# Kernel tuning notes

Measured on AMD Instinct MI355X. Metric: run time of the kernel, lower is better.

Reference implementation:

```python
import jax, jax.numpy as jnp
import numpy as np

N = 10000          # num token nodes
E = 320000         # num token-token edges (avg degree 32)
IN_DIM = 512
FEAT_DIM = 128
OUT_DIM = 64       # per-head dim
HEADS = 8
NEG_SLOPE = 0.01   # torch F.leaky_relu default


def setup_inputs() -> dict:
    key = jax.random.key(0)
    k = jax.random.split(key, 7)
    h = jax.random.normal(k[0], (N, IN_DIM), dtype=jnp.float32)
    dep_emb = jax.random.normal(k[1], (E, FEAT_DIM), dtype=jnp.float32)
    src = jax.random.randint(k[2], (E,), 0, N, dtype=jnp.int32)
    dst = jnp.sort(jax.random.randint(k[3], (E,), 0, N, dtype=jnp.int32))
    # xavier-normal-ish init (gain for relu ~ sqrt(2))
    w_fc = jax.random.normal(k[4], (IN_DIM, OUT_DIM * HEADS), dtype=jnp.float32) * np.float32(np.sqrt(4.0 / (IN_DIM + OUT_DIM * HEADS)))
    w_feat = jax.random.normal(k[5], (FEAT_DIM, OUT_DIM * HEADS), dtype=jnp.float32) * np.float32(np.sqrt(4.0 / (FEAT_DIM + OUT_DIM * HEADS)))
    w_attn = jax.random.normal(k[6], (3 * OUT_DIM,), dtype=jnp.float32) * np.float32(np.sqrt(4.0 / (3 * OUT_DIM + 1)))
    return {"h": h, "dep_emb": dep_emb, "src": src, "dst": dst,
            "w_fc": w_fc, "w_feat": w_feat, "w_attn": w_attn}


def reference(h, dep_emb, src, dst, w_fc, w_feat, w_attn):
    # node projection: [N, H, D]
    z = (h @ w_fc).reshape(N, HEADS, OUT_DIM)
    # edge-feature projection: [E, H, D]
    feat = (dep_emb @ w_feat).reshape(E, HEADS, OUT_DIM)
    # attn_fc on concat([z_src, z_dst, feat]) == sum of three dot products
    a_src, a_dst, a_feat = jnp.split(w_attn, 3)
    node_src_score = jnp.einsum('nhd,d->nh', z, a_src)  # [N, H]
    node_dst_score = jnp.einsum('nhd,d->nh', z, a_dst)  # [N, H]
    e = node_src_score[src] + node_dst_score[dst] + jnp.einsum('ehd,d->eh', feat, a_feat)  # [E, H]
    e = jnp.where(e >= 0, e, NEG_SLOPE * e)  # leaky_relu
    # segment softmax over incoming edges of each dst node
    m = jax.ops.segment_max(e, dst, num_segments=N)           # [N, H]
    m = jnp.where(jnp.isfinite(m), m, jnp.zeros_like(m))      # empty segments
    ex = jnp.exp(e - m[dst])                                  # [E, H]
    denom = jax.ops.segment_sum(ex, dst, num_segments=N)      # [N, H]
    alpha = ex / jnp.maximum(denom[dst], 1e-30)               # [E, H]
    # scatter weighted sum of source features back to dst nodes
    out = jax.ops.segment_sum(alpha[:, :, None] * z[src], dst, num_segments=N)  # [N, H, D]
    return out
```

## Files before the change

### kernel.cpp

```cpp
#include <hip/hip_runtime.h>
#include <math.h>

#define NN 10000
#define NPAD 10112
#define NE 320000
#define IN_DIM 512
#define FEAT_DIM 128
#define OD 64
#define NH 8
#define ZD 512
#define NEG 0.01f

typedef __attribute__((ext_vector_type(8))) __bf16 bf16x8;
typedef __attribute__((ext_vector_type(4))) float f32x4;

__device__ __forceinline__ unsigned short f2b(float f) {
  __bf16 b = (__bf16)f;
  return __builtin_bit_cast(unsigned short, b);
}
__device__ __forceinline__ float blo(unsigned int v) {
  unsigned int x = v << 16;
  return __builtin_bit_cast(float, x);
}
__device__ __forceinline__ float bhi(unsigned int v) {
  unsigned int x = v & 0xFFFF0000u;
  return __builtin_bit_cast(float, x);
}

__device__ __forceinline__ void gload16(const void* g, void* l) {
  __builtin_amdgcn_global_load_lds((const __attribute__((address_space(1))) unsigned int*)g,
                                   (__attribute__((address_space(3))) unsigned int*)l, 16, 0, 0);
}

#define PREP_H2B 2528
#define PREP_WT  (PREP_H2B + 256)
#define PREP_WFA (PREP_WT + 8)
#define PREP_ALL (PREP_WFA + 40)
__global__ __launch_bounds__(256) void k_prep(const float* __restrict__ h,
    const float* __restrict__ w_fc, const float* __restrict__ w_feat,
    const float* __restrict__ w_attn, const int* __restrict__ dst,
    unsigned short* __restrict__ hb, unsigned short* __restrict__ wt,
    unsigned short* __restrict__ wfab, int* __restrict__ row_start) {
  const int bid = blockIdx.x, t = threadIdx.x;
  if (bid < PREP_H2B) {
    size_t base = ((size_t)bid * 256 + t) * 8;
    int row = (int)(base >> 9);
    ushort4 o0, o1;
    if (row < NN) {
      float4 v0 = *(const float4*)(h + base);
      float4 v1 = *(const float4*)(h + base + 4);
      o0 = make_ushort4(f2b(v0.x), f2b(v0.y), f2b(v0.z), f2b(v0.w));
      o1 = make_ushort4(f2b(v1.x), f2b(v1.y), f2b(v1.z), f2b(v1.w));
    } else {
      o0 = make_ushort4(0, 0, 0, 0);
      o1 = make_ushort4(0, 0, 0, 0);
    }
    *(ushort4*)(hb + base) = o0;
    *(ushort4*)(hb + base + 4) = o1;
  } else if (bid < PREP_WT) {
    __shared__ float tile[32][33];
    const int b2 = bid - PREP_H2B;
    const int tx = (b2 & 15) * 32, ty = (b2 >> 4) * 32;
    const int r = t >> 3, c4 = (t & 7) * 4;
    float4 v = *(const float4*)(w_fc + (size_t)(ty + r) * ZD + tx + c4);
    tile[r][c4 + 0] = v.x; tile[r][c4 + 1] = v.y; tile[r][c4 + 2] = v.z; tile[r][c4 + 3] = v.w;
    __syncthreads();
    ushort4 o = make_ushort4(f2b(tile[c4 + 0][r]), f2b(tile[c4 + 1][r]),
                             f2b(tile[c4 + 2][r]), f2b(tile[c4 + 3][r]));
    *(ushort4*)(wt + (size_t)(tx + r) * IN_DIM + ty + c4) = o;
  } else if (bid < PREP_WFA) {
    int tid = (bid - PREP_WT) * 256 + t;
    if (tid < FEAT_DIM * NH) {
      int f = tid >> 3, hh = tid & 7;
      const float* wr = w_feat + (size_t)f * ZD + hh * OD;
      const float* a  = w_attn + 2 * OD;
      float s = 0.f;
      #pragma unroll 8
      for (int d = 0; d < OD; ++d) s += wr[d] * a[d];
      wfab[hh * FEAT_DIM + f] = f2b(s);
    } else if (tid < 2 * FEAT_DIM * NH) {
      wfab[tid] = 0;
    }
  } else {
    int n = (bid - PREP_WFA) * 256 + t;
    if (n <= NN) {
      int lo = 0, hi = NE;
      while (lo < hi) { int mid = (lo + hi) >> 1; if (dst[mid] < n) lo = mid + 1; else hi = mid; }
      row_start[n] = lo;
    }
  }
}

#define GEMM_BLOCKS 316
__global__ __launch_bounds__(256) void k_fused(const unsigned short* __restrict__ A,
    const unsigned short* __restrict__ Bt, const float* __restrict__ w_attn,
    const float* __restrict__ dep_emb, const unsigned short* __restrict__ wfab,
    unsigned short* __restrict__ zb, float* __restrict__ s_src,
    float* __restrict__ s_dst, float* __restrict__ e_feat) {
  __shared__ __align__(16) char smem[16384];
  const int bid = blockIdx.x, t = threadIdx.x;
  const int lane = t & 63, wave = t >> 6;
  const int fr = lane & 15, kq = lane >> 4;

  if (bid < GEMM_BLOCKS) {
    unsigned short* As = (unsigned short*)smem;
    unsigned short* Bs = (unsigned short*)(smem + 8192);
    const int m0 = (bid % 79) * 128;
    const int n0 = (bid / 79) * 128;
    const int wr = (wave >> 1) * 64, wc = (wave & 1) * 64;

    f32x4 acc[4][4] = {};

    const int idx0 = t, idx1 = t + 256;
    const unsigned short* ga0 = A + (size_t)(m0 + (idx0 & 127)) * IN_DIM + (idx0 >> 7) * 8;
    const unsigned short* ga1 = A + (size_t)(m0 + (idx1 & 127)) * IN_DIM + (idx1 >> 7) * 8;
    const unsigned short* gb0 = Bt + (size_t)(n0 + (idx0 & 127)) * IN_DIM + (idx0 >> 7) * 8;
    const unsigned short* gb1 = Bt + (size_t)(n0 + (idx1 & 127)) * IN_DIM + (idx1 >> 7) * 8;
    unsigned short* la0 = &As[idx0 * 8];
    unsigned short* la1 = &As[idx1 * 8];
    unsigned short* lb0 = &Bs[idx0 * 8];
    unsigned short* lb1 = &Bs[idx1 * 8];

    for (int k0 = 0; k0 < IN_DIM; k0 += 32) {
      gload16(ga0 + k0, la0);
      gload16(ga1 + k0, la1);
      gload16(gb0 + k0, lb0);
      gload16(gb1 + k0, lb1);
      __syncthreads();
      bf16x8 a[4], b[4];
      #pragma unroll
      for (int m = 0; m < 4; m++)
        a[m] = *(const bf16x8*)&As[(kq * 128 + wr + m * 16 + fr) * 8];
      #pragma unroll
      for (int n = 0; n < 4; n++)
        b[n] = *(const bf16x8*)&Bs[(kq * 128 + wc + n * 16 + fr) * 8];
      #pragma unroll
      for (int m = 0; m < 4; m++)
        #pragma unroll
        for (int n = 0; n < 4; n++)
          acc[m][n] = __builtin_amdgcn_mfma_f32_16x16x32_bf16(a[m], b[n], acc[m][n], 0, 0, 0);
      __syncthreads();
    }

    float as_[4], ad_[4];
    #pragma unroll
    for (int n = 0; n < 4; n++) {
      as_[n] = w_attn[n * 16 + fr];
      ad_[n] = w_attn[OD + n * 16 + fr];
    }
    const int crow = kq * 4;
    const int ccol = lane & 15;
    const int hh = (n0 + wc) >> 6;

    #pragma unroll
    for (int m = 0; m < 4; m++) {
      #pragma unroll
      for (int n = 0; n < 4; n++) {
        int row = m0 + wr + m * 16 + crow;
        int col = n0 + wc + n * 16 + ccol;
        #pragma unroll
        for (int j = 0; j < 4; j++)
          if (row + j < NN) zb[(size_t)(row + j) * ZD + col] = f2b(acc[m][n][j]);
      }
      float sp[4] = {0.f, 0.f, 0.f, 0.f}, sd[4] = {0.f, 0.f, 0.f, 0.f};
      #pragma unroll
      for (int n = 0; n < 4; n++)
        #pragma unroll
        for (int j = 0; j < 4; j++) {
          sp[j] = fmaf(acc[m][n][j], as_[n], sp[j]);
          sd[j] = fmaf(acc[m][n][j], ad_[n], sd[j]);
        }
      #pragma unroll
      for (int o = 1; o < 16; o <<= 1)
        #pragma unroll
        for (int j = 0; j < 4; j++) {
          sp[j] += __shfl_xor(sp[j], o);
          sd[j] += __shfl_xor(sd[j], o);
        }
      if (fr == 0) {
        int row = m0 + wr + m * 16 + crow;
        #pragma unroll
        for (int j = 0; j < 4; j++)
          if (row + j < NN) {
            s_src[(size_t)(row + j) * NH + hh] = sp[j];
            s_dst[(size_t)(row + j) * NH + hh] = sd[j];
          }
      }
    }
  } else {
    const int erow = (bid - GEMM_BLOCKS) * 64 + wave * 16 + fr;
    const float* arow = dep_emb + (size_t)erow * FEAT_DIM;
    f32x4 acc = {};
    #pragma unroll
    for (int kk = 0; kk < 4; kk++) {
      float4 v0 = *(const float4*)(arow + kk * 32 + kq * 8);
      float4 v1 = *(const float4*)(arow + kk * 32 + kq * 8 + 4);
      bf16x8 a;
      a[0] = (__bf16)v0.x; a[1] = (__bf16)v0.y; a[2] = (__bf16)v0.z; a[3] = (__bf16)v0.w;
      a[4] = (__bf16)v1.x; a[5] = (__bf16)v1.y; a[6] = (__bf16)v1.z; a[7] = (__bf16)v1.w;
      bf16x8 b = *(const bf16x8*)&wfab[fr * FEAT_DIM + kk * 32 + kq * 8];
      acc = __builtin_amdgcn_mfma_f32_16x16x32_bf16(a, b, acc, 0, 0, 0);
    }
    if (fr < NH) {
      const int ebase = (bid - GEMM_BLOCKS) * 64 + wave * 16 + kq * 4;
      #pragma unroll
      for (int j = 0; j < 4; j++)
        e_feat[(size_t)(ebase + j) * NH + fr] = acc[j];
    }
  }
}

#define CH2 64
__global__ __launch_bounds__(256) void k_agg(const float* __restrict__ ef,
    const int* __restrict__ src, const int* __restrict__ row_start,
    const float* __restrict__ s_src, const float* __restrict__ s_dst,
    const unsigned short* __restrict__ zb, float* __restrict__ out) {
  __shared__ float els[4 * CH2 * NH];
  __shared__ int   src_s[4 * CH2];
  const int t = threadIdx.x;
  const int w = t >> 6, l = t & 63;
  const int n = blockIdx.x * 4 + w;
  const int es = l >> 3;
  const int hs = l & 7;
  const int hc = l >> 3;
  float* myels = els + w * (CH2 * NH);
  int*   mysrc = src_s + w * CH2;

  const int start = row_start[n], end = row_start[n + 1];
  const float sdn = s_dst[(size_t)n * NH + hs];
  float m = -INFINITY, den = 0.f;
  float acc_e[8] = {0.f,0.f,0.f,0.f,0.f,0.f,0.f,0.f};
  float acc_o[8] = {0.f,0.f,0.f,0.f,0.f,0.f,0.f,0.f};
  const unsigned short* zcol = zb + l * 8;

  for (int c0 = start; c0 < end; c0 += CH2) {
    const int cn = min(CH2, end - c0);
    if (l < cn) mysrc[l] = src[c0 + l];
    float e_r[CH2 / 8];
    float mchunk = -INFINITY;
    #pragma unroll
    for (int p = 0; p < CH2 / 8; p++) {
      int i = p * 8 + es;
      float e = -INFINITY;
      if (i < cn) {
        int sid = mysrc[i];
        e = ef[(size_t)(c0 + i) * NH + hs] + s_src[(size_t)sid * NH + hs] + sdn;
        e = e >= 0.f ? e : NEG * e;
      }
      e_r[p] = e;
      mchunk = fmaxf(mchunk, e);
    }
    mchunk = fmaxf(mchunk, __shfl_xor(mchunk, 8));
    mchunk = fmaxf(mchunk, __shfl_xor(mchunk, 16));
    mchunk = fmaxf(mchunk, __shfl_xor(mchunk, 32));
    float mn = fmaxf(m, mchunk);
    float dc = 0.f;
    #pragma unroll
    for (int p = 0; p < CH2 / 8; p++) {
      float ex = __expf(e_r[p] - mn);
      dc += ex;
      myels[(p * 8 + es) * NH + hs] = ex;
    }
    dc += __shfl_xor(dc, 8);
    dc += __shfl_xor(dc, 16);
    dc += __shfl_xor(dc, 32);
    float rs = __expf(m - mn);
    den = den * rs + dc;
    m = mn;
    float rs_c = __shfl(rs, hc);
    #pragma unroll
    for (int j = 0; j < 8; j++) { acc_e[j] *= rs_c; acc_o[j] *= rs_c; }
    int i = 0;
    for (; i + 4 <= cn; i += 4) {
      int s0 = mysrc[i], s1 = mysrc[i + 1], s2 = mysrc[i + 2], s3 = mysrc[i + 3];
      float w0 = myels[i * NH + hc];
      float w1 = myels[(i + 1) * NH + hc];
      float w2 = myels[(i + 2) * NH + hc];
      float w3 = myels[(i + 3) * NH + hc];
      uint4 u0 = *(const uint4*)(zcol + ((size_t)s0 << 9));
      uint4 u1 = *(const uint4*)(zcol + ((size_t)s1 << 9));
      uint4 u2 = *(const uint4*)(zcol + ((size_t)s2 << 9));
      uint4 u3 = *(const uint4*)(zcol + ((size_t)s3 << 9));
      acc_e[0] = fmaf(w0, blo(u0.x), acc_e[0]); acc_e[1] = fmaf(w0, bhi(u0.x), acc_e[1]);
      acc_e[2] = fmaf(w0, blo(u0.y), acc_e[2]); acc_e[3] = fmaf(w0, bhi(u0.y), acc_e[3]);
      acc_e[4] = fmaf(w0, blo(u0.z), acc_e[4]); acc_e[5] = fmaf(w0, bhi(u0.z), acc_e[5]);
      acc_e[6] = fmaf(w0, blo(u0.w), acc_e[6]); acc_e[7] = fmaf(w0, bhi(u0.w), acc_e[7]);
      acc_o[0] = fmaf(w1, blo(u1.x), acc_o[0]); acc_o[1] = fmaf(w1, bhi(u1.x), acc_o[1]);
      acc_o[2] = fmaf(w1, blo(u1.y), acc_o[2]); acc_o[3] = fmaf(w1, bhi(u1.y), acc_o[3]);
      acc_o[4] = fmaf(w1, blo(u1.z), acc_o[4]); acc_o[5] = fmaf(w1, bhi(u1.z), acc_o[5]);
      acc_o[6] = fmaf(w1, blo(u1.w), acc_o[6]); acc_o[7] = fmaf(w1, bhi(u1.w), acc_o[7]);
      acc_e[0] = fmaf(w2, blo(u2.x), acc_e[0]); acc_e[1] = fmaf(w2, bhi(u2.x), acc_e[1]);
      acc_e[2] = fmaf(w2, blo(u2.y), acc_e[2]); acc_e[3] = fmaf(w2, bhi(u2.y), acc_e[3]);
      acc_e[4] = fmaf(w2, blo(u2.z), acc_e[4]); acc_e[5] = fmaf(w2, bhi(u2.z), acc_e[5]);
      acc_e[6] = fmaf(w2, blo(u2.w), acc_e[6]); acc_e[7] = fmaf(w2, bhi(u2.w), acc_e[7]);
      acc_o[0] = fmaf(w3, blo(u3.x), acc_o[0]); acc_o[1] = fmaf(w3, bhi(u3.x), acc_o[1]);
      acc_o[2] = fmaf(w3, blo(u3.y), acc_o[2]); acc_o[3] = fmaf(w3, bhi(u3.y), acc_o[3]);
      acc_o[4] = fmaf(w3, blo(u3.z), acc_o[4]); acc_o[5] = fmaf(w3, bhi(u3.z), acc_o[5]);
      acc_o[6] = fmaf(w3, blo(u3.w), acc_o[6]); acc_o[7] = fmaf(w3, bhi(u3.w), acc_o[7]);
    }
    for (; i < cn; i++) {
      int s0 = mysrc[i];
      float w0 = myels[i * NH + hc];
      uint4 u0 = *(const uint4*)(zcol + ((size_t)s0 << 9));
      acc_e[0] = fmaf(w0, blo(u0.x), acc_e[0]); acc_e[1] = fmaf(w0, bhi(u0.x), acc_e[1]);
      acc_e[2] = fmaf(w0, blo(u0.y), acc_e[2]); acc_e[3] = fmaf(w0, bhi(u0.y), acc_e[3]);
      acc_e[4] = fmaf(w0, blo(u0.z), acc_e[4]); acc_e[5] = fmaf(w0, bhi(u0.z), acc_e[5]);
      acc_e[6] = fmaf(w0, blo(u0.w), acc_e[6]); acc_e[7] = fmaf(w0, bhi(u0.w), acc_e[7]);
    }
  }
  float den_c = __shfl(den, hc);
  float inv = den_c > 0.f ? 1.f / den_c : 0.f;
  float4 o0, o1;
  o0.x = (acc_e[0] + acc_o[0]) * inv; o0.y = (acc_e[1] + acc_o[1]) * inv;
  o0.z = (acc_e[2] + acc_o[2]) * inv; o0.w = (acc_e[3] + acc_o[3]) * inv;
  o1.x = (acc_e[4] + acc_o[4]) * inv; o1.y = (acc_e[5] + acc_o[5]) * inv;
  o1.z = (acc_e[6] + acc_o[6]) * inv; o1.w = (acc_e[7] + acc_o[7]) * inv;
  float* orow = out + (size_t)n * ZD + l * 8;
  *(float4*)orow = o0;
  *(float4*)(orow + 4) = o1;
}

extern "C" void kernel_launch(void* const* d_in, const int* in_sizes, int n_in,
                              void* d_out, int out_size, void* d_ws, size_t ws_size,
                              hipStream_t stream) {
  const float* h      = (const float*)d_in[0];
  const float* dep    = (const float*)d_in[1];
  const int*   src    = (const int*)d_in[2];
  const int*   dst    = (const int*)d_in[3];
  const float* w_fc   = (const float*)d_in[4];
  const float* w_feat = (const float*)d_in[5];
  const float* w_attn = (const float*)d_in[6];
  float* out = (float*)d_out;

  char* ws = (char*)d_ws;
  size_t off = 0;
  auto alloc = [&](size_t bytes) { void* p = ws + off; off = (off + bytes + 63) & ~(size_t)63; return p; };
  float* s_src  = (float*)alloc((size_t)NN * NH * 4);
  float* s_dst  = (float*)alloc((size_t)NN * NH * 4);
  float* e_feat = (float*)alloc((size_t)NE * NH * 4);
  unsigned short* wfab = (unsigned short*)alloc(2 * FEAT_DIM * NH * 2);
  int*   row_st = (int*)alloc((NN + 2) * 4);
  unsigned short* zb = (unsigned short*)alloc((size_t)NN * ZD * 2);
  unsigned short* hb = (unsigned short*)alloc((size_t)NPAD * IN_DIM * 2);
  unsigned short* wt = (unsigned short*)alloc((size_t)IN_DIM * ZD * 2);

  k_prep <<<PREP_ALL, 256, 0, stream>>>(h, w_fc, w_feat, w_attn, dst, hb, wt, wfab, row_st);
  k_fused<<<GEMM_BLOCKS + NE / 64, 256, 0, stream>>>(hb, wt, w_attn, dep, wfab,
                                                     zb, s_src, s_dst, e_feat);
  k_agg  <<<NN / 4, 256, 0, stream>>>(e_feat, src, row_st, s_src, s_dst, zb, out);
}
```

Baseline: 97.65 us.

## Split each destination node's aggregation across four waves with block-level reductions

```diff
diff --git a/kernel.cpp b/kernel.cpp
--- a/kernel.cpp
+++ b/kernel.cpp
@@ -210,114 +210,129 @@
   }
 }
 
-#define CH2 64
+#define CH3 64
 __global__ __launch_bounds__(256) void k_agg(const float* __restrict__ ef,
     const int* __restrict__ src, const int* __restrict__ row_start,
     const float* __restrict__ s_src, const float* __restrict__ s_dst,
     const unsigned short* __restrict__ zb, float* __restrict__ out) {
-  __shared__ float els[4 * CH2 * NH];
-  __shared__ int   src_s[4 * CH2];
+  __shared__ float els[CH3 * NH];
+  __shared__ int   src_s[CH3];
+  __shared__ float hmax[4][NH];
+  __shared__ float hsum[4][NH];
+  __shared__ float dsh[NH];
+  __shared__ float red[4][ZD];
+
+  const int n = blockIdx.x;
   const int t = threadIdx.x;
   const int w = t >> 6, l = t & 63;
-  const int n = blockIdx.x * 4 + w;
-  const int es = l >> 3;
   const int hs = l & 7;
+  const int e8 = l >> 3;
   const int hc = l >> 3;
-  float* myels = els + w * (CH2 * NH);
-  int*   mysrc = src_s + w * CH2;
 
   const int start = row_start[n], end = row_start[n + 1];
   const float sdn = s_dst[(size_t)n * NH + hs];
   float m = -INFINITY, den = 0.f;
-  float acc_e[8] = {0.f,0.f,0.f,0.f,0.f,0.f,0.f,0.f};
-  float acc_o[8] = {0.f,0.f,0.f,0.f,0.f,0.f,0.f,0.f};
+  float acc[8] = {0.f,0.f,0.f,0.f,0.f,0.f,0.f,0.f};
   const unsigned short* zcol = zb + l * 8;
 
-  for (int c0 = start; c0 < end; c0 += CH2) {
-    const int cn = min(CH2, end - c0);
-    if (l < cn) mysrc[l] = src[c0 + l];
-    float e_r[CH2 / 8];
-    float mchunk = -INFINITY;
-    #pragma unroll
-    for (int p = 0; p < CH2 / 8; p++) {
-      int i = p * 8 + es;
+  for (int c0 = start; c0 < end; c0 += CH3) {
+    const int cn = min(CH3, end - c0);
+    if (t < cn) src_s[t] = src[c0 + t];
+    __syncthreads();
+    float e_r[2];
+    float mc = -INFINITY;
+    #pragma unroll
+    for (int p = 0; p < 2; p++) {
+      int i = w * 16 + p * 8 + e8;
       float e = -INFINITY;
       if (i < cn) {
-        int sid = mysrc[i];
-        e = ef[(size_t)(c0 + i) * NH + hs] + s_src[(size_t)sid * NH + hs] + sdn;
-        e = e >= 0.f ? e : NEG * e;
+        int sid = src_s[i];
+        float f = ef[(size_t)(c0 + i) * NH + hs] + s_src[(size_t)sid * NH + hs] + sdn;
+        e = f >= 0.f ? f : NEG * f;
       }
       e_r[p] = e;
-      mchunk = fmaxf(mchunk, e);
-    }
-    mchunk = fmaxf(mchunk, __shfl_xor(mchunk, 8));
-    mchunk = fmaxf(mchunk, __shfl_xor(mchunk, 16));
-    mchunk = fmaxf(mchunk, __shfl_xor(mchunk, 32));
-    float mn = fmaxf(m, mchunk);
-    float dc = 0.f;
-    #pragma unroll
-    for (int p = 0; p < CH2 / 8; p++) {
-      float ex = __expf(e_r[p] - mn);
-      dc += ex;
-      myels[(p * 8 + es) * NH + hs] = ex;
-    }
-    dc += __shfl_xor(dc, 8);
-    dc += __shfl_xor(dc, 16);
-    dc += __shfl_xor(dc, 32);
+      mc = fmaxf(mc, e);
+    }
+    mc = fmaxf(mc, __shfl_xor(mc, 8));
+    mc = fmaxf(mc, __shfl_xor(mc, 16));
+    mc = fmaxf(mc, __shfl_xor(mc, 32));
+    if (l < NH) hmax[w][l] = mc;
+    __syncthreads();
+    float mcb = fmaxf(fmaxf(hmax[0][hs], hmax[1][hs]), fmaxf(hmax[2][hs], hmax[3][hs]));
+    float mn = fmaxf(m, mcb);
+    float sc = 0.f;
+    #pragma unroll
+    for (int p = 0; p < 2; p++) {
+      int i = w * 16 + p * 8 + e8;
+      float x = __expf(e_r[p] - mn);
+      sc += x;
+      if (i < cn) els[i * NH + hs] = x;
+    }
+    sc += __shfl_xor(sc, 8);
+    sc += __shfl_xor(sc, 16);
+    sc += __shfl_xor(sc, 32);
+    if (l < NH) hsum[w][l] = sc;
+    __syncthreads();
+    float scb = hsum[0][hs] + hsum[1][hs] + hsum[2][hs] + hsum[3][hs];
     float rs = __expf(m - mn);
-    den = den * rs + dc;
+    den = den * rs + scb;
     m = mn;
     float rs_c = __shfl(rs, hc);
     #pragma unroll
-    for (int j = 0; j < 8; j++) { acc_e[j] *= rs_c; acc_o[j] *= rs_c; }
-    int i = 0;
-    for (; i + 4 <= cn; i += 4) {
-      int s0 = mysrc[i], s1 = mysrc[i + 1], s2 = mysrc[i + 2], s3 = mysrc[i + 3];
-      float w0 = myels[i * NH + hc];
-      float w1 = myels[(i + 1) * NH + hc];
-      float w2 = myels[(i + 2) * NH + hc];
-      float w3 = myels[(i + 3) * NH + hc];
+    for (int j = 0; j < 8; j++) acc[j] *= rs_c;
+    const int lo = w * 16;
+    const int hi = min(lo + 16, cn);
+    int i = lo;
+    for (; i + 4 <= hi; i += 4) {
+      int s0 = src_s[i], s1 = src_s[i + 1], s2 = src_s[i + 2], s3 = src_s[i + 3];
+      float w0 = els[i * NH + hc];
+      float w1 = els[(i + 1) * NH + hc];
+      float w2 = els[(i + 2) * NH + hc];
+      float w3 = els[(i + 3) * NH + hc];
       uint4 u0 = *(const uint4*)(zcol + ((size_t)s0 << 9));
       uint4 u1 = *(const uint4*)(zcol + ((size_t)s1 << 9));
       uint4 u2 = *(const uint4*)(zcol + ((size_t)s2 << 9));
       uint4 u3 = *(const uint4*)(zcol + ((size_t)s3 << 9));
-      acc_e[0] = fmaf(w0, blo(u0.x), acc_e[0]); acc_e[1] = fmaf(w0, bhi(u0.x), acc_e[1]);
-      acc_e[2] = fmaf(w0, blo(u0.y), acc_e[2]); acc_e[3] = fmaf(w0, bhi(u0.y), acc_e[3]);
-      acc_e[4] = fmaf(w0, blo(u0.z), acc_e[4]); acc_e[5] = fmaf(w0, bhi(u0.z), acc_e[5]);
-      acc_e[6] = fmaf(w0, blo(u0.w), acc_e[6]); acc_e[7] = fmaf(w0, bhi(u0.w), acc_e[7]);
-      acc_o[0] = fmaf(w1, blo(u1.x), acc_o[0]); acc_o[1] = fmaf(w1, bhi(u1.x), acc_o[1]);
-      acc_o[2] = fmaf(w1, blo(u1.y), acc_o[2]); acc_o[3] = fmaf(w1, bhi(u1.y), acc_o[3]);
-      acc_o[4] = fmaf(w1, blo(u1.z), acc_o[4]); acc_o[5] = fmaf(w1, bhi(u1.z), acc_o[5]);
-      acc_o[6] = fmaf(w1, blo(u1.w), acc_o[6]); acc_o[7] = fmaf(w1, bhi(u1.w), acc_o[7]);
-      acc_e[0] = fmaf(w2, blo(u2.x), acc_e[0]); acc_e[1] = fmaf(w2, bhi(u2.x), acc_e[1]);
-      acc_e[2] = fmaf(w2, blo(u2.y), acc_e[2]); acc_e[3] = fmaf(w2, bhi(u2.y), acc_e[3]);
-      acc_e[4] = fmaf(w2, blo(u2.z), acc_e[4]); acc_e[5] = fmaf(w2, bhi(u2.z), acc_e[5]);
-      acc_e[6] = fmaf(w2, blo(u2.w), acc_e[6]); acc_e[7] = fmaf(w2, bhi(u2.w), acc_e[7]);
-      acc_o[0] = fmaf(w3, blo(u3.x), acc_o[0]); acc_o[1] = fmaf(w3, bhi(u3.x), acc_o[1]);
-      acc_o[2] = fmaf(w3, blo(u3.y), acc_o[2]); acc_o[3] = fmaf(w3, bhi(u3.y), acc_o[3]);
-      acc_o[4] = fmaf(w3, blo(u3.z), acc_o[4]); acc_o[5] = fmaf(w3, bhi(u3.z), acc_o[5]);
-      acc_o[6] = fmaf(w3, blo(u3.w), acc_o[6]); acc_o[7] = fmaf(w3, bhi(u3.w), acc_o[7]);
-    }
-    for (; i < cn; i++) {
-      int s0 = mysrc[i];
-      float w0 = myels[i * NH + hc];
+      acc[0] = fmaf(w0, blo(u0.x), acc[0]); acc[1] = fmaf(w0, bhi(u0.x), acc[1]);
+      acc[2] = fmaf(w0, blo(u0.y), acc[2]); acc[3] = fmaf(w0, bhi(u0.y), acc[3]);
+      acc[4] = fmaf(w0, blo(u0.z), acc[4]); acc[5] = fmaf(w0, bhi(u0.z), acc[5]);
+      acc[6] = fmaf(w0, blo(u0.w), acc[6]); acc[7] = fmaf(w0, bhi(u0.w), acc[7]);
+      acc[0] = fmaf(w1, blo(u1.x), acc[0]); acc[1] = fmaf(w1, bhi(u1.x), acc[1]);
+      acc[2] = fmaf(w1, blo(u1.y), acc[2]); acc[3] = fmaf(w1, bhi(u1.y), acc[3]);
+      acc[4] = fmaf(w1, blo(u1.z), acc[4]); acc[5] = fmaf(w1, bhi(u1.z), acc[5]);
+      acc[6] = fmaf(w1, blo(u1.w), acc[6]); acc[7] = fmaf(w1, bhi(u1.w), acc[7]);
+      acc[0] = fmaf(w2, blo(u2.x), acc[0]); acc[1] = fmaf(w2, bhi(u2.x), acc[1]);
+      acc[2] = fmaf(w2, blo(u2.y), acc[2]); acc[3] = fmaf(w2, bhi(u2.y), acc[3]);
+      acc[4] = fmaf(w2, blo(u2.z), acc[4]); acc[5] = fmaf(w2, bhi(u2.z), acc[5]);
+      acc[6] = fmaf(w2, blo(u2.w), acc[6]); acc[7] = fmaf(w2, bhi(u2.w), acc[7]);
+      acc[0] = fmaf(w3, blo(u3.x), acc[0]); acc[1] = fmaf(w3, bhi(u3.x), acc[1]);
+      acc[2] = fmaf(w3, blo(u3.y), acc[2]); acc[3] = fmaf(w3, bhi(u3.y), acc[3]);
+      acc[4] = fmaf(w3, blo(u3.z), acc[4]); acc[5] = fmaf(w3, bhi(u3.z), acc[5]);
+      acc[6] = fmaf(w3, blo(u3.w), acc[6]); acc[7] = fmaf(w3, bhi(u3.w), acc[7]);
+    }
+    for (; i < hi; i++) {
+      int s0 = src_s[i];
+      float w0 = els[i * NH + hc];
       uint4 u0 = *(const uint4*)(zcol + ((size_t)s0 << 9));
-      acc_e[0] = fmaf(w0, blo(u0.x), acc_e[0]); acc_e[1] = fmaf(w0, bhi(u0.x), acc_e[1]);
-      acc_e[2] = fmaf(w0, blo(u0.y), acc_e[2]); acc_e[3] = fmaf(w0, bhi(u0.y), acc_e[3]);
-      acc_e[4] = fmaf(w0, blo(u0.z), acc_e[4]); acc_e[5] = fmaf(w0, bhi(u0.z), acc_e[5]);
-      acc_e[6] = fmaf(w0, blo(u0.w), acc_e[6]); acc_e[7] = fmaf(w0, bhi(u0.w), acc_e[7]);
-    }
+      acc[0] = fmaf(w0, blo(u0.x), acc[0]); acc[1] = fmaf(w0, bhi(u0.x), acc[1]);
+      acc[2] = fmaf(w0, blo(u0.y), acc[2]); acc[3] = fmaf(w0, bhi(u0.y), acc[3]);
+      acc[4] = fmaf(w0, blo(u0.z), acc[4]); acc[5] = fmaf(w0, bhi(u0.z), acc[5]);
+      acc[6] = fmaf(w0, blo(u0.w), acc[6]); acc[7] = fmaf(w0, bhi(u0.w), acc[7]);
+    }
+    __syncthreads();
   }
-  float den_c = __shfl(den, hc);
-  float inv = den_c > 0.f ? 1.f / den_c : 0.f;
-  float4 o0, o1;
-  o0.x = (acc_e[0] + acc_o[0]) * inv; o0.y = (acc_e[1] + acc_o[1]) * inv;
-  o0.z = (acc_e[2] + acc_o[2]) * inv; o0.w = (acc_e[3] + acc_o[3]) * inv;
-  o1.x = (acc_e[4] + acc_o[4]) * inv; o1.y = (acc_e[5] + acc_o[5]) * inv;
-  o1.z = (acc_e[6] + acc_o[6]) * inv; o1.w = (acc_e[7] + acc_o[7]) * inv;
-  float* orow = out + (size_t)n * ZD + l * 8;
-  *(float4*)orow = o0;
-  *(float4*)(orow + 4) = o1;
+
+  #pragma unroll
+  for (int j = 0; j < 8; j++) red[w][l * 8 + j] = acc[j];
+  if (w == 0 && l < NH) dsh[l] = den;
+  __syncthreads();
+  const int c = t * 2;
+  float dd = dsh[t >> 5];
+  float inv = dd > 0.f ? 1.f / dd : 0.f;
+  float2 o;
+  o.x = (red[0][c]     + red[1][c]     + red[2][c]     + red[3][c])     * inv;
+  o.y = (red[0][c + 1] + red[1][c + 1] + red[2][c + 1] + red[3][c + 1]) * inv;
+  *(float2*)&out[(size_t)n * ZD + c] = o;
 }
 
 extern "C" void kernel_launch(void* const* d_in, const int* in_sizes, int n_in,
@@ -347,5 +362,5 @@
   k_prep <<<PREP_ALL, 256, 0, stream>>>(h, w_fc, w_feat, w_attn, dst, hb, wt, wfab, row_st);
   k_fused<<<GEMM_BLOCKS + NE / 64, 256, 0, stream>>>(hb, wt, w_attn, dep, wfab,
                                                      zb, s_src, s_dst, e_feat);
-  k_agg  <<<NN / 4, 256, 0, stream>>>(e_feat, src, row_st, s_src, s_dst, zb, out);
-}
+  k_agg  <<<NN, 256, 0, stream>>>(e_feat, src, row_st, s_src, s_dst, zb, out);
+}
```

Result: slower. 106.4 us (+9.0%).
